# Kernel tuning notes

Measured on AMD Instinct MI355X. Metric: run time of the kernel, lower is better.

## Reference

```python
import jax, jax.numpy as jnp
import numpy as np

B, C, H, W = 4, 256, 64, 64
C8, C2 = C // 8, C // 2


def _conv(x, w, b):
    # NCHW conv with SAME padding
    y = jax.lax.conv_general_dilated(x, w, (1, 1), 'SAME',
                                     dimension_numbers=('NCHW', 'OIHW', 'NCHW'))
    return y + b[None, :, None, None]


def _bn(x, s, bi, m, v):
    # eval-mode batchnorm, eps matches torch default 1e-5
    inv = jax.lax.rsqrt(v + 1e-5)
    return (x - m[None, :, None, None]) * (inv * s)[None, :, None, None] + bi[None, :, None, None]


def setup_inputs() -> dict:
    ks = jax.random.split(jax.random.key(0), 8)
    return {
        'x': jax.random.normal(ks[0], (B, C, H, W), jnp.float32),
        'q_w': jax.random.normal(ks[1], (C8, C, 3, 3), jnp.float32) * 0.02,
        'q_b': jnp.zeros((C8,), jnp.float32),
        'q_bn_s': jnp.ones((C8,), jnp.float32),
        'q_bn_b': jnp.zeros((C8,), jnp.float32),
        'q_bn_m': jnp.zeros((C8,), jnp.float32),
        'q_bn_v': jnp.ones((C8,), jnp.float32),
        'k_w': jax.random.normal(ks[2], (C8, C, 3, 3), jnp.float32) * 0.02,
        'k_b': jnp.zeros((C8,), jnp.float32),
        'k_bn_s': jnp.ones((C8,), jnp.float32),
        'k_bn_b': jnp.zeros((C8,), jnp.float32),
        'k_bn_m': jnp.zeros((C8,), jnp.float32),
        'k_bn_v': jnp.ones((C8,), jnp.float32),
        'v_w': jax.random.normal(ks[3], (C, C), jnp.float32) * 0.02,
        'v_b': jnp.zeros((C,), jnp.float32),
        'gamma': jnp.full((1,), 0.5, jnp.float32),
        'c_w1': jax.random.normal(ks[4], (C2, C), jnp.float32) * 0.02,
        'c_b1': jnp.zeros((C2,), jnp.float32),
        'c_w2': jax.random.normal(ks[5], (C, C2), jnp.float32) * 0.02,
        'c_b2': jnp.zeros((C,), jnp.float32),
        's_vw': jax.random.normal(ks[6], (C, C), jnp.float32) * 0.02,
        's_vb': jnp.zeros((C,), jnp.float32),
        's_cw': jax.random.normal(ks[7], (1, 2, 3, 3), jnp.float32) * 0.1,
        's_cb': jnp.zeros((1,), jnp.float32),
        's_bn_s': jnp.ones((1,), jnp.float32),
        's_bn_b': jnp.zeros((1,), jnp.float32),
        's_bn_m': jnp.zeros((1,), jnp.float32),
        's_bn_v': jnp.ones((1,), jnp.float32),
    }


def reference(x, q_w, q_b, q_bn_s, q_bn_b, q_bn_m, q_bn_v,
              k_w, k_b, k_bn_s, k_bn_b, k_bn_m, k_bn_v,
              v_w, v_b, gamma, c_w1, c_b1, c_w2, c_b2,
              s_vw, s_vb, s_cw, s_cb, s_bn_s, s_bn_b, s_bn_m, s_bn_v):
    Bn, Cn, Hn, Wn = x.shape
    HW = Hn * Wn

    # ---- SelfAttention branch ----
    q = jax.nn.relu(_bn(_conv(x, q_w, q_b), q_bn_s, q_bn_b, q_bn_m, q_bn_v)).reshape(Bn, -1, HW)  # [B,C8,HW]
    k = jax.nn.relu(_bn(_conv(x, k_w, k_b), k_bn_s, k_bn_b, k_bn_m, k_bn_v)).reshape(Bn, -1, HW)  # [B,C8,HW]
    aff = jax.nn.softmax(jnp.einsum('bcn,bcm->bnm', q, k), axis=-1)  # [B,HW,HW]
    v = (jnp.einsum('bchw,oc->bohw', x, v_w) + v_b[None, :, None, None]).reshape(Bn, Cn, HW)
    wts = jnp.einsum('bcm,bnm->bcn', v, aff).reshape(Bn, Cn, Hn, Wn)
    selfA = gamma * wts + x

    # ---- Channel mean/max attention ----
    def fc(s):  # s: [B,C]
        h = jax.nn.relu(s @ c_w1.T + c_b1)
        return h @ c_w2.T + c_b2

    gate = jax.nn.sigmoid(fc(x.mean((2, 3))) + fc(x.max((2, 3))))  # [B,C]
    channelA = x * gate[:, :, None, None]

    # ---- Spatial mean/max attention ----
    v2 = jnp.einsum('bchw,oc->bohw', x, s_vw) + s_vb[None, :, None, None]  # [B,C,H,W]
    sm = jnp.stack([v2.max(1), v2.mean(1)], axis=1)  # [B,2,H,W]
    a = _bn(_conv(sm, s_cw, s_cb), s_bn_s, s_bn_b, s_bn_m, s_bn_v)  # [B,1,H,W]
    a = jax.nn.softmax(a[:, 0], axis=-1)  # [B,H,W], softmax over W
    spatialA = jnp.einsum('bchw,bwk->bchk', x, a)  # batched matmul, needs H==W

    return selfA + channelA + spatialA
```

## Files before the change

### kernel.cpp

```cpp
#include <hip/hip_runtime.h>
#include <math.h>

#define NB 4
#define NC 256
#define NHW 4096
#define NC8 32
#define NC2 128

typedef unsigned short u16;
typedef __attribute__((ext_vector_type(8))) short s8v;
typedef __attribute__((ext_vector_type(4))) short s4v;
typedef __attribute__((ext_vector_type(4))) float f4v;

__device__ __forceinline__ u16 f2bf(float x) {
    unsigned int u = __builtin_bit_cast(unsigned int, x);
    u += 0x7FFFu + ((u >> 16) & 1u);
    return (u16)(u >> 16);
}
__device__ __forceinline__ float bf2f(u16 h) {
    unsigned int u = ((unsigned int)h) << 16;
    return __builtin_bit_cast(float, u);
}
__device__ __forceinline__ s8v ld_sp(const u16* p) {
    s4v a = *(const s4v*)p;
    s4v b = *(const s4v*)(p + 4);
    return __builtin_shufflevector(a, b, 0, 1, 2, 3, 4, 5, 6, 7);
}

#define MFMA16(a, b, c) __builtin_amdgcn_mfma_f32_16x16x32_bf16((a), (b), (c), 0, 0, 0)

__global__ __launch_bounds__(256) void k_conv_qk(
    const float* __restrict__ x,
    const float* __restrict__ qw, const float* __restrict__ kw,
    float* __restrict__ part)
{
    __shared__ float plane[2][64 * 65];
    const int cog = blockIdx.x;
    const int cic = blockIdx.y;
    const int b   = blockIdx.z;
    const int t   = threadIdx.x;
    const int co0 = cog * 4;
    const bool isq = co0 < NC8;
    const int oc0 = isq ? co0 : co0 - NC8;
    const float* wsel = isq ? qw : kw;
    const int ci0 = cic * 64;
    const int r  = t >> 2;
    const int c0 = (t & 3) * 16;
    float acc[4][16];
#pragma unroll
    for (int j = 0; j < 4; ++j)
#pragma unroll
        for (int q = 0; q < 16; ++q) acc[j][q] = 0.f;

    const float* xb = x + (size_t)b * NC * NHW;
    float4 pf[4];
    {
        const float4* src = (const float4*)(xb + (size_t)ci0 * NHW);
#pragma unroll
        for (int u = 0; u < 4; ++u) pf[u] = src[t + 256 * u];
    }
    for (int ci = ci0; ci < ci0 + 64; ++ci) {
        const int cur = ci & 1;
#pragma unroll
        for (int u = 0; u < 4; ++u) {
            int g  = (t + 256 * u) << 2;
            int rr = g >> 6, cc = g & 63;
            float* p = &plane[cur][rr * 65 + cc];
            p[0] = pf[u].x; p[1] = pf[u].y; p[2] = pf[u].z; p[3] = pf[u].w;
        }
        __syncthreads();
        if (ci + 1 < ci0 + 64) {
            const float4* src = (const float4*)(xb + (size_t)(ci + 1) * NHW);
#pragma unroll
            for (int u = 0; u < 4; ++u) pf[u] = src[t + 256 * u];
        }
        float w9[4][9];
#pragma unroll
        for (int j = 0; j < 4; ++j)
#pragma unroll
            for (int u = 0; u < 9; ++u)
                w9[j][u] = wsel[((size_t)(oc0 + j) * NC + ci) * 9 + u];
#pragma unroll
        for (int dy = 0; dy < 3; ++dy) {
            int rr = r + dy - 1;
            if (rr >= 0 && rr <= 63) {
                const float* row = &plane[cur][rr * 65];
                float tv[18];
#pragma unroll
                for (int jj = 0; jj < 18; ++jj) {
                    int cc = c0 + jj - 1;
                    tv[jj] = (cc >= 0 && cc < 64) ? row[cc] : 0.f;
                }
#pragma unroll
                for (int j = 0; j < 4; ++j) {
                    float wa = w9[j][dy * 3 + 0], wb = w9[j][dy * 3 + 1], wc = w9[j][dy * 3 + 2];
#pragma unroll
                    for (int q = 0; q < 16; ++q)
                        acc[j][q] += wa * tv[q] + wb * tv[q + 1] + wc * tv[q + 2];
                }
            }
        }
        __syncthreads();
    }
    float* pp = part + (((size_t)(cic * 4 + b) * 64 + co0) * NHW) + r * 64 + c0;
#pragma unroll
    for (int j = 0; j < 4; ++j)
#pragma unroll
        for (int q4 = 0; q4 < 4; ++q4) {
            float4 o;
            o.x = acc[j][q4 * 4 + 0]; o.y = acc[j][q4 * 4 + 1];
            o.z = acc[j][q4 * 4 + 2]; o.w = acc[j][q4 * 4 + 3];
            *(float4*)(pp + (size_t)j * NHW + q4 * 4) = o;
        }
}

__global__ __launch_bounds__(256) void k_qk_finish(
    const float* __restrict__ part,
    const float* __restrict__ qb, const float* __restrict__ qbs, const float* __restrict__ qbb,
    const float* __restrict__ qbm, const float* __restrict__ qbv,
    const float* __restrict__ kb, const float* __restrict__ kbs, const float* __restrict__ kbb,
    const float* __restrict__ kbm, const float* __restrict__ kbv,
    u16* __restrict__ qh, u16* __restrict__ ql,
    u16* __restrict__ kh, u16* __restrict__ kl)
{
    const int t = threadIdx.x;
    const int b = blockIdx.y;
    const int n = blockIdx.x * 64 + (t & 63);
    const int coq = t >> 6;
    const int cb2 = coq * 16;
    float s[16];
#pragma unroll
    for (int j = 0; j < 16; ++j) s[j] = 0.f;
#pragma unroll
    for (int cic = 0; cic < 4; ++cic)
#pragma unroll
        for (int j = 0; j < 16; ++j)
            s[j] += part[(((size_t)(cic * 4 + b)) * 64 + cb2 + j) * NHW + n];
    const bool isq = coq < 2;
    u16 hi[16], lo[16];
#pragma unroll
    for (int j = 0; j < 16; ++j) {
        int oc = (coq & 1) * 16 + j;
        float cbv = isq ? qb[oc]  : kb[oc];
        float sv  = isq ? qbs[oc] : kbs[oc];
        float bbv = isq ? qbb[oc] : kbb[oc];
        float mv  = isq ? qbm[oc] : kbm[oc];
        float vv  = isq ? qbv[oc] : kbv[oc];
        float inv = rsqrtf(vv + 1e-5f);
        float scale = inv * sv;
        float shift = (cbv - mv) * scale + bbv;
        float y = fmaxf(s[j] * scale + shift, 0.f);
        hi[j] = f2bf(y);
        lo[j] = f2bf(y - bf2f(hi[j]));
    }
    u16* dh = isq ? qh : kh;
    u16* dl = isq ? ql : kl;
    size_t base = ((size_t)b * NHW + n) * 32 + (coq & 1) * 16;
    uint4 ph0, ph1, pl0, pl1;
    ph0.x = (unsigned)hi[0]  | ((unsigned)hi[1]  << 16);
    ph0.y = (unsigned)hi[2]  | ((unsigned)hi[3]  << 16);
    ph0.z = (unsigned)hi[4]  | ((unsigned)hi[5]  << 16);
    ph0.w = (unsigned)hi[6]  | ((unsigned)hi[7]  << 16);
    ph1.x = (unsigned)hi[8]  | ((unsigned)hi[9]  << 16);
    ph1.y = (unsigned)hi[10] | ((unsigned)hi[11] << 16);
    ph1.z = (unsigned)hi[12] | ((unsigned)hi[13] << 16);
    ph1.w = (unsigned)hi[14] | ((unsigned)hi[15] << 16);
    pl0.x = (unsigned)lo[0]  | ((unsigned)lo[1]  << 16);
    pl0.y = (unsigned)lo[2]  | ((unsigned)lo[3]  << 16);
    pl0.z = (unsigned)lo[4]  | ((unsigned)lo[5]  << 16);
    pl0.w = (unsigned)lo[6]  | ((unsigned)lo[7]  << 16);
    pl1.x = (unsigned)lo[8]  | ((unsigned)lo[9]  << 16);
    pl1.y = (unsigned)lo[10] | ((unsigned)lo[11] << 16);
    pl1.z = (unsigned)lo[12] | ((unsigned)lo[13] << 16);
    pl1.w = (unsigned)lo[14] | ((unsigned)lo[15] << 16);
    *(uint4*)&dh[base]     = ph0;
    *(uint4*)&dh[base + 8] = ph1;
    *(uint4*)&dl[base]     = pl0;
    *(uint4*)&dl[base + 8] = pl1;
}

__global__ __launch_bounds__(256) void k_gemm_vv2(
    const float* __restrict__ x,
    const float* __restrict__ vw, const float* __restrict__ vb,
    const float* __restrict__ sw, const float* __restrict__ sb,
    float* __restrict__ v2T, u16* __restrict__ vhi, u16* __restrict__ vlo)
{
    __shared__ float Ax[16 * 68];
    __shared__ float Bw1[16 * 68];
    __shared__ float Bw2[16 * 68];
    const int t  = threadIdx.x;
    const int n0 = blockIdx.x * 64;
    const int o0 = blockIdx.y * 64;
    const int b  = blockIdx.z;
    const int ni = t & 15, oi = t >> 4;
    float a1[4][4], a2[4][4];
#pragma unroll
    for (int i = 0; i < 4; ++i)
#pragma unroll
        for (int j = 0; j < 4; ++j) { a1[i][j] = 0.f; a2[i][j] = 0.f; }

    const int sk  = t >> 4;
    const int sf  = t & 15;
    const int so  = t & 63;
    const int skq = t >> 6;
    const float* xb = x + ((size_t)b * NC) * NHW + n0;

    float4 ax = *(const float4*)(xb + (size_t)sk * NHW + sf * 4);
    float4 f1 = *(const float4*)(vw + (size_t)(o0 + so) * NC + skq * 4);
    float4 f2 = *(const float4*)(sw + (size_t)(o0 + so) * NC + skq * 4);

    for (int c0 = 0; c0 < NC; c0 += 16) {
        *(float4*)&Ax[sk * 68 + sf * 4] = ax;
        Bw1[(skq * 4 + 0) * 68 + so] = f1.x;
        Bw1[(skq * 4 + 1) * 68 + so] = f1.y;
        Bw1[(skq * 4 + 2) * 68 + so] = f1.z;
        Bw1[(skq * 4 + 3) * 68 + so] = f1.w;
        Bw2[(skq * 4 + 0) * 68 + so] = f2.x;
        Bw2[(skq * 4 + 1) * 68 + so] = f2.y;
        Bw2[(skq * 4 + 2) * 68 + so] = f2.z;
        Bw2[(skq * 4 + 3) * 68 + so] = f2.w;
        __syncthreads();
        if (c0 + 16 < NC) {
            ax = *(const float4*)(xb + (size_t)(c0 + 16 + sk) * NHW + sf * 4);
            f1 = *(const float4*)(vw + (size_t)(o0 + so) * NC + c0 + 16 + skq * 4);
            f2 = *(const float4*)(sw + (size_t)(o0 + so) * NC + c0 + 16 + skq * 4);
        }
#pragma unroll
        for (int k = 0; k < 16; ++k) {
            float4 af = *(const float4*)&Ax[k * 68 + ni * 4];
            float4 g1 = *(const float4*)&Bw1[k * 68 + oi * 4];
            float4 g2 = *(const float4*)&Bw2[k * 68 + oi * 4];
            const float* ap = (const float*)&af;
            const float* p1 = (const float*)&g1;
            const float* p2 = (const float*)&g2;
#pragma unroll
            for (int i = 0; i < 4; ++i)
#pragma unroll
                for (int j = 0; j < 4; ++j) {
                    a1[i][j] += ap[i] * p1[j];
                    a2[i][j] += ap[i] * p2[j];
                }
        }
        __syncthreads();
    }
    float vb4[4], sb4[4];
#pragma unroll
    for (int j = 0; j < 4; ++j) { vb4[j] = vb[o0 + oi * 4 + j]; sb4[j] = sb[o0 + oi * 4 + j]; }
#pragma unroll
    for (int i = 0; i < 4; ++i) {
        size_t idx = ((size_t)b * NHW + n0 + ni * 4 + i) * NC + o0 + oi * 4;
        float4 o2v;
        o2v.x = a2[i][0] + sb4[0]; o2v.y = a2[i][1] + sb4[1];
        o2v.z = a2[i][2] + sb4[2]; o2v.w = a2[i][3] + sb4[3];
        *(float4*)&v2T[idx] = o2v;
    }
#pragma unroll
    for (int j = 0; j < 4; ++j) {
        u16 h[4], l[4];
#pragma unroll
        for (int i = 0; i < 4; ++i) {
            float y = a1[i][j] + vb4[j];
            h[i] = f2bf(y);
            l[i] = f2bf(y - bf2f(h[i]));
        }
        size_t vi = ((size_t)b * NC + o0 + oi * 4 + j) * NHW + n0 + ni * 4;
        uint2 uh, ul;
        uh.x = (unsigned)h[0] | ((unsigned)h[1] << 16);
        uh.y = (unsigned)h[2] | ((unsigned)h[3] << 16);
        ul.x = (unsigned)l[0] | ((unsigned)l[1] << 16);
        ul.y = (unsigned)l[2] | ((unsigned)l[3] << 16);
        *(uint2*)&vhi[vi] = uh;
        *(uint2*)&vlo[vi] = ul;
    }
}

__global__ __launch_bounds__(256) void k_reduce_v2(const float* __restrict__ v2T,
                                                   float* __restrict__ smo)
{
    const int t = threadIdx.x;
    const int lane = t & 63, wv = t >> 6;
    const int row = blockIdx.x * 4 + wv;
    float4 f = ((const float4*)(v2T + (size_t)row * NC))[lane];
    float mx = fmaxf(fmaxf(f.x, f.y), fmaxf(f.z, f.w));
    float sm = f.x + f.y + f.z + f.w;
#pragma unroll
    for (int off = 32; off; off >>= 1) {
        mx = fmaxf(mx, __shfl_down(mx, off));
        sm += __shfl_down(sm, off);
    }
    if (lane == 0) {
        int b = row >> 12, n = row & 4095;
        smo[((size_t)b * 2 + 0) * NHW + n] = mx;
        smo[((size_t)b * 2 + 1) * NHW + n] = sm * (1.f / NC);
    }
}

__global__ __launch_bounds__(256) void k_spatial(
    const float* __restrict__ smo, const float* __restrict__ scw,
    const float* __restrict__ scb, const float* __restrict__ sbs,
    const float* __restrict__ sbb2, const float* __restrict__ sbm,
    const float* __restrict__ sbv, float* __restrict__ Amat)
{
    __shared__ float ch[2][64 * 68];
    __shared__ float lg[64 * 68];
    const int t = threadIdx.x;
    const int b = blockIdx.x;
#pragma unroll
    for (int u = 0; u < 8; ++u) {
        int g  = t + 256 * u;
        int c  = g >> 10, gi = g & 1023;
        int row = gi >> 4, col4 = (gi & 15) * 4;
        float4 f = ((const float4*)(smo + ((size_t)b * 2 + c) * NHW))[gi];
        *(float4*)&ch[c][row * 68 + col4] = f;
    }
    __syncthreads();
    float w9[2][9];
#pragma unroll
    for (int ic = 0; ic < 2; ++ic)
#pragma unroll
        for (int j = 0; j < 9; ++j) w9[ic][j] = scw[ic * 9 + j];
    float A0, Bsh;
    {
        float inv = rsqrtf(sbv[0] + 1e-5f);
        A0  = inv * sbs[0];
        Bsh = (scb[0] - sbm[0]) * A0 + sbb2[0];
    }
#pragma unroll
    for (int u = 0; u < 16; ++u) {
        int px = t + 256 * u;
        int h = px >> 6, w = px & 63;
        float acc = 0.f;
#pragma unroll
        for (int ic = 0; ic < 2; ++ic)
#pragma unroll
            for (int dy = 0; dy < 3; ++dy) {
                int rr = h + dy - 1;
                if (rr < 0 || rr > 63) continue;
#pragma unroll
                for (int dx = 0; dx < 3; ++dx) {
                    int cc = w + dx - 1;
                    if (cc < 0 || cc > 63) continue;
                    acc += w9[ic][dy * 3 + dx] * ch[ic][rr * 68 + cc];
                }
            }
        lg[h * 68 + w] = acc * A0 + Bsh;
    }
    __syncthreads();
    if (t < 64) {
        float M = -INFINITY;
        for (int k2 = 0; k2 < 64; ++k2) M = fmaxf(M, lg[t * 68 + k2]);
        float L = 0.f;
        for (int k2 = 0; k2 < 64; ++k2) L += __expf(lg[t * 68 + k2] - M);
        float rli = 1.f / L;
        for (int k2 = 0; k2 < 64; ++k2)
            Amat[(size_t)b * NHW + t * 64 + k2] = __expf(lg[t * 68 + k2] - M) * rli;
    }
}

__global__ __launch_bounds__(256) void k_xstats(const float* __restrict__ x,
                                                float* __restrict__ smean,
                                                float* __restrict__ smax)
{
    const int t = threadIdx.x;
    const int c = blockIdx.x, b = blockIdx.y;
    const float* row = x + ((size_t)b * NC + c) * NHW;
    float s = 0.f, m = -INFINITY;
#pragma unroll
    for (int u = 0; u < 4; ++u) {
        float4 f = ((const float4*)row)[t + 256 * u];
        s += f.x + f.y + f.z + f.w;
        m = fmaxf(m, fmaxf(fmaxf(f.x, f.y), fmaxf(f.z, f.w)));
    }
    __shared__ float red[8];
    const int lane = t & 63, wv = t >> 6;
#pragma unroll
    for (int off = 32; off; off >>= 1) {
        s += __shfl_down(s, off);
        m = fmaxf(m, __shfl_down(m, off));
    }
    if (lane == 0) { red[wv] = s; red[4 + wv] = m; }
    __syncthreads();
    if (t == 0) {
        float S = red[0] + red[1] + red[2] + red[3];
        float M = fmaxf(fmaxf(red[4], red[5]), fmaxf(red[6], red[7]));
        smean[b * NC + c] = S * (1.f / NHW);
        smax[b * NC + c]  = M;
    }
}

__global__ __launch_bounds__(256) void k_gate(
    const float* __restrict__ smean, const float* __restrict__ smax,
    const float* __restrict__ w1, const float* __restrict__ b1,
    const float* __restrict__ w2, const float* __restrict__ b2,
    float* __restrict__ gate)
{
    __shared__ float smL[256], sxL[256], hL[256];
    const int t = threadIdx.x;
    const int b = blockIdx.x;
    smL[t] = smean[b * NC + t];
    sxL[t] = smax[b * NC + t];
    __syncthreads();
    {
        const int j = t & 127;
        const float* in = (t < 128) ? smL : sxL;
        const float* wr = w1 + (size_t)j * NC;
        float acc = b1[j];
        for (int c = 0; c < NC; c += 4) {
            float4 f = *(const float4*)(wr + c);
            acc += f.x * in[c] + f.y * in[c + 1] + f.z * in[c + 2] + f.w * in[c + 3];
        }
        hL[t] = fmaxf(acc, 0.f);
    }
    __syncthreads();
    {
        const float* wr = w2 + (size_t)t * NC2;
        float acc = 2.f * b2[t];
        for (int j = 0; j < NC2; j += 4) {
            float4 f = *(const float4*)(wr + j);
            acc += f.x * (hL[j]     + hL[128 + j])
                 + f.y * (hL[j + 1] + hL[129 + j])
                 + f.z * (hL[j + 2] + hL[130 + j])
                 + f.w * (hL[j + 3] + hL[131 + j]);
        }
        gate[b * NC + t] = 1.f / (1.f + __expf(-acc));
    }
}

__global__ __launch_bounds__(64) void k_softstats(
    const u16* __restrict__ qh, const u16* __restrict__ ql,
    const u16* __restrict__ kh, const u16* __restrict__ kl,
    float* __restrict__ mx, float* __restrict__ rl)
{
    const int t  = threadIdx.x;
    const int li = t & 15, g = t >> 4;
    const int n0 = blockIdx.x * 16;
    const int b  = blockIdx.y;
    const size_t qoff = ((size_t)b * NHW + n0 + li) * 32 + g * 8;
    const s8v qfh = *(const s8v*)&qh[qoff];
    const s8v qfl = *(const s8v*)&ql[qoff];
    const size_t kb0 = ((size_t)b * NHW + li) * 32 + g * 8;
    s8v ka0 = *(const s8v*)&kh[kb0];
    s8v ka1 = *(const s8v*)&kh[kb0 + 512];
    s8v la0 = *(const s8v*)&kl[kb0];
    s8v la1 = *(const s8v*)&kl[kb0 + 512];
    float mrun = -INFINITY, lrun = 0.f;
    for (int it = 0; it < 128; ++it) {
        f4v c0 = {0.f, 0.f, 0.f, 0.f}, c1 = {0.f, 0.f, 0.f, 0.f};
        c0 = MFMA16(ka0, qfh, c0); c0 = MFMA16(ka0, qfl, c0); c0 = MFMA16(la0, qfh, c0);
        c1 = MFMA16(ka1, qfh, c1); c1 = MFMA16(ka1, qfl, c1); c1 = MFMA16(la1, qfh, c1);
        if (it + 1 < 128) {
            size_t o = kb0 + (size_t)(it + 1) * 1024;
            ka0 = *(const s8v*)&kh[o];
            ka1 = *(const s8v*)&kh[o + 512];
            la0 = *(const s8v*)&kl[o];
            la1 = *(const s8v*)&kl[o + 512];
        }
        float tmax = fmaxf(fmaxf(fmaxf(c0[0], c0[1]), fmaxf(c0[2], c0[3])),
                           fmaxf(fmaxf(c1[0], c1[1]), fmaxf(c1[2], c1[3])));
        tmax = fmaxf(tmax, __shfl_xor(tmax, 16));
        tmax = fmaxf(tmax, __shfl_xor(tmax, 32));
        float nm = fmaxf(mrun, tmax);
        float ls = 0.f;
#pragma unroll
        for (int r = 0; r < 4; ++r) ls += __expf(c0[r] - nm);
#pragma unroll
        for (int r = 0; r < 4; ++r) ls += __expf(c1[r] - nm);
        ls += __shfl_xor(ls, 16);
        ls += __shfl_xor(ls, 32);
        lrun = lrun * __expf(mrun - nm) + ls;
        mrun = nm;
    }
    if (g == 0) {
        mx[(size_t)b * NHW + n0 + li] = mrun;
        rl[(size_t)b * NHW + n0 + li] = 1.f / lrun;
    }
}

__global__ __launch_bounds__(256, 2) void k_flash(
    const u16* __restrict__ qh, const u16* __restrict__ ql,
    const u16* __restrict__ kh, const u16* __restrict__ kl,
    const u16* __restrict__ vhi, const u16* __restrict__ vlo,
    const float* __restrict__ mx, const float* __restrict__ rl,
    float* __restrict__ w0, float* __restrict__ w1)
{
    __shared__ __align__(16) u16 Sp[2][4][16 * 36];
    const int t = threadIdx.x;
    const int bid = blockIdx.x;
    const int v   = (bid & 7) * 64 + (bid >> 3);
    const int n0  = (v & 63) * 64;
    const int mh  = (v >> 6) & 1;
    const int b   = v >> 7;
    const int mbase = mh * 2048;
    const int li = t & 15, g = (t >> 4) & 3, wv = t >> 6;

    const size_t qoff = ((size_t)b * NHW + n0 + wv * 16 + li) * 32 + g * 8;
    const s8v qfh = *(const s8v*)&qh[qoff];
    const s8v qfl = *(const s8v*)&ql[qoff];
    const float mxv = mx[(size_t)b * NHW + n0 + wv * 16 + li];
    const float rlv = rl[(size_t)b * NHW + n0 + wv * 16 + li];

    f4v acc[4][4];
#pragma unroll
    for (int i = 0; i < 4; ++i)
#pragma unroll
        for (int j = 0; j < 4; ++j) { f4v z = {0.f, 0.f, 0.f, 0.f}; acc[i][j] = z; }

    const size_t kb0 = ((size_t)b * NHW + mbase + li) * 32 + g * 8;
    s8v ka0 = *(const s8v*)&kh[kb0];
    s8v ka1 = *(const s8v*)&kh[kb0 + 512];
    s8v la0 = *(const s8v*)&kl[kb0];
    s8v la1 = *(const s8v*)&kl[kb0 + 512];

    const size_t vb0 = ((size_t)b * NC + wv * 64 + li) * NHW + mbase + g * 8;
    s8v vfh[4], vfl[4];
#pragma unroll
    for (int ct = 0; ct < 4; ++ct) {
        vfh[ct] = *(const s8v*)&vhi[vb0 + (size_t)ct * 16 * NHW];
        vfl[ct] = *(const s8v*)&vlo[vb0 + (size_t)ct * 16 * NHW];
    }

    for (int it = 0; it < 64; ++it) {
        f4v c0 = {0.f, 0.f, 0.f, 0.f}, c1 = {0.f, 0.f, 0.f, 0.f};
        c0 = MFMA16(ka0, qfh, c0); c0 = MFMA16(ka0, qfl, c0); c0 = MFMA16(la0, qfh, c0);
        c1 = MFMA16(ka1, qfh, c1); c1 = MFMA16(ka1, qfl, c1); c1 = MFMA16(la1, qfh, c1);
        {
            size_t o = kb0 + (size_t)(it + 1) * 1024;
            ka0 = *(const s8v*)&kh[o];
            ka1 = *(const s8v*)&kh[o + 512];
            la0 = *(const s8v*)&kl[o];
            la1 = *(const s8v*)&kl[o + 512];
        }
        u16 h0[4], h1[4];
#pragma unroll
        for (int r = 0; r < 4; ++r) {
            h0[r] = f2bf(__expf(c0[r] - mxv) * rlv);
            h1[r] = f2bf(__expf(c1[r] - mxv) * rlv);
        }
        u16* sp = &Sp[it & 1][wv][0];
        uint2 uw0, uw1;
        uw0.x = (unsigned)h0[0] | ((unsigned)h0[1] << 16);
        uw0.y = (unsigned)h0[2] | ((unsigned)h0[3] << 16);
        uw1.x = (unsigned)h1[0] | ((unsigned)h1[1] << 16);
        uw1.y = (unsigned)h1[2] | ((unsigned)h1[3] << 16);
        *(uint2*)&sp[li * 36 + g * 4]      = uw0;
        *(uint2*)&sp[li * 36 + 16 + g * 4] = uw1;
        __syncthreads();
        s8v pa0 = ld_sp(&Sp[it & 1][0][li * 36 + g * 8]);
        s8v pa1 = ld_sp(&Sp[it & 1][1][li * 36 + g * 8]);
        s8v pa2 = ld_sp(&Sp[it & 1][2][li * 36 + g * 8]);
        s8v pa3 = ld_sp(&Sp[it & 1][3][li * 36 + g * 8]);
#pragma unroll
        for (int ct = 0; ct < 4; ++ct) {
            acc[0][ct] = MFMA16(pa0, vfh[ct], acc[0][ct]);
            acc[0][ct] = MFMA16(pa0, vfl[ct], acc[0][ct]);
            acc[1][ct] = MFMA16(pa1, vfh[ct], acc[1][ct]);
            acc[1][ct] = MFMA16(pa1, vfl[ct], acc[1][ct]);
            acc[2][ct] = MFMA16(pa2, vfh[ct], acc[2][ct]);
            acc[2][ct] = MFMA16(pa2, vfl[ct], acc[2][ct]);
            acc[3][ct] = MFMA16(pa3, vfh[ct], acc[3][ct]);
            acc[3][ct] = MFMA16(pa3, vfl[ct], acc[3][ct]);
        }
        {
            size_t o = vb0 + (size_t)(it + 1) * 32;
#pragma unroll
            for (int ct = 0; ct < 4; ++ct) {
                vfh[ct] = *(const s8v*)&vhi[o + (size_t)ct * 16 * NHW];
                vfl[ct] = *(const s8v*)&vlo[o + (size_t)ct * 16 * NHW];
            }
        }
    }
    float* wout = (mh == 0) ? w0 : w1;
#pragma unroll
    for (int ng = 0; ng < 4; ++ng)
#pragma unroll
        for (int ct = 0; ct < 4; ++ct)
#pragma unroll
            for (int r = 0; r < 4; ++r)
                wout[((size_t)b * NHW + n0 + ng * 16 + g * 4 + r) * NC
                     + wv * 64 + ct * 16 + li] = acc[ng][ct][r];
}

__global__ __launch_bounds__(256) void k_final(
    const float* __restrict__ x, const float* __restrict__ w0,
    const float* __restrict__ w1, const float* __restrict__ gate,
    const float* __restrict__ Amat, const float* __restrict__ gamma,
    float* __restrict__ out)
{
    __shared__ float As[64 * 65];
    __shared__ float xs[64 * 65];
    const int t = threadIdx.x;
    const int h = blockIdx.x, b = blockIdx.y;
    const float g0 = gamma[0];
    const int kq = t >> 4;
    const int cq = t & 15;
#pragma unroll
    for (int u = 0; u < 4; ++u) {
        int gidx = t + 256 * u;
        int w = gidx >> 4, k4 = (gidx & 15) * 4;
        float4 f = ((const float4*)(Amat + (size_t)b * NHW))[gidx];
        *(float4*)&As[w * 65 + k4] = f;
    }
    for (int ch = 0; ch < 4; ++ch) {
        __syncthreads();
#pragma unroll
        for (int u = 0; u < 4; ++u) {
            int gidx = t + 256 * u;
            int c = gidx >> 4, w4 = (gidx & 15) * 4;
            float4 f = *(const float4*)(x + ((size_t)(b * NC) + ch * 64 + c) * NHW + h * 64 + w4);
            xs[(w4 + 0) * 65 + c] = f.x;
            xs[(w4 + 1) * 65 + c] = f.y;
            xs[(w4 + 2) * 65 + c] = f.z;
            xs[(w4 + 3) * 65 + c] = f.w;
        }
        __syncthreads();
        float acc[4][4];
#pragma unroll
        for (int i = 0; i < 4; ++i)
#pragma unroll
            for (int j = 0; j < 4; ++j) acc[i][j] = 0.f;
        for (int w = 0; w < 64; ++w) {
            float4 av = *(const float4*)&As[w * 65 + kq * 4];
            float4 xv = *(const float4*)&xs[w * 65 + cq * 4];
            const float* ap = (const float*)&av;
            const float* xp = (const float*)&xv;
#pragma unroll
            for (int i = 0; i < 4; ++i)
#pragma unroll
                for (int j = 0; j < 4; ++j)
                    acc[i][j] += xp[i] * ap[j];
        }
#pragma unroll
        for (int i = 0; i < 4; ++i) {
            const int c = ch * 64 + cq * 4 + i;
            const float gt1 = 1.f + gate[b * NC + c];
#pragma unroll
            for (int j = 0; j < 4; ++j) {
                const int k = kq * 4 + j;
                const int n = h * 64 + k;
                const float xv = xs[k * 65 + cq * 4 + i];
                const size_t widx = ((size_t)b * NHW + n) * NC + c;
                const float wsum = w0[widx] + w1[widx];
                out[((size_t)(b * NC + c)) * NHW + n] = g0 * wsum + xv * gt1 + acc[i][j];
            }
        }
    }
}

extern "C" void kernel_launch(void* const* d_in, const int* in_sizes, int n_in,
                              void* d_out, int out_size, void* d_ws, size_t ws_size,
                              hipStream_t stream)
{
    const float* x    = (const float*)d_in[0];
    const float* qw   = (const float*)d_in[1];
    const float* qb   = (const float*)d_in[2];
    const float* qbs  = (const float*)d_in[3];
    const float* qbb  = (const float*)d_in[4];
    const float* qbm  = (const float*)d_in[5];
    const float* qbv  = (const float*)d_in[6];
    const float* kw   = (const float*)d_in[7];
    const float* kb   = (const float*)d_in[8];
    const float* kbs  = (const float*)d_in[9];
    const float* kbb  = (const float*)d_in[10];
    const float* kbm  = (const float*)d_in[11];
    const float* kbv  = (const float*)d_in[12];
    const float* vw   = (const float*)d_in[13];
    const float* vb   = (const float*)d_in[14];
    const float* gm   = (const float*)d_in[15];
    const float* cw1  = (const float*)d_in[16];
    const float* cb1  = (const float*)d_in[17];
    const float* cw2  = (const float*)d_in[18];
    const float* cb2  = (const float*)d_in[19];
    const float* svw  = (const float*)d_in[20];
    const float* svb  = (const float*)d_in[21];
    const float* scw  = (const float*)d_in[22];
    const float* scb  = (const float*)d_in[23];
    const float* sbs  = (const float*)d_in[24];
    const float* sbb  = (const float*)d_in[25];
    const float* sbm  = (const float*)d_in[26];
    const float* sbv  = (const float*)d_in[27];

    float* ws    = (float*)d_ws;
    float* part  = ws;
    float* w0    = ws;
    float* v2T   = ws + 4194304;
    float* w1    = ws + 4194304;
    u16*   vhi   = (u16*)(ws + 8388608);
    u16*   vlo   = (u16*)(ws + 10485760);
    u16*   qhB   = (u16*)(ws + 12582912);
    u16*   qlB   = (u16*)(ws + 12845056);
    u16*   khB   = (u16*)(ws + 13107200);
    u16*   klB   = (u16*)(ws + 13369344);
    float* mxp   = ws + 13631488;
    float* rlp   = ws + 13647872;
    float* smean = ws + 13664256;
    float* smax  = ws + 13665280;
    float* gate  = ws + 13666304;
    float* smo   = ws + 13667328;
    float* Amat  = ws + 13700096;

    k_conv_qk  <<<dim3(16, 4, NB), 256, 0, stream>>>(x, qw, kw, part);
    k_qk_finish<<<dim3(64, NB),    256, 0, stream>>>(part, qb, qbs, qbb, qbm, qbv,
                                                     kb, kbs, kbb, kbm, kbv,
                                                     qhB, qlB, khB, klB);
    k_gemm_vv2 <<<dim3(64, 4, NB), 256, 0, stream>>>(x, vw, vb, svw, svb, v2T, vhi, vlo);
    k_reduce_v2<<<dim3(4096),      256, 0, stream>>>(v2T, smo);
    k_spatial  <<<dim3(NB),        256, 0, stream>>>(smo, scw, scb, sbs, sbb, sbm, sbv, Amat);
    k_xstats   <<<dim3(NC, NB),    256, 0, stream>>>(x, smean, smax);
    k_gate     <<<dim3(NB),        256, 0, stream>>>(smean, smax, cw1, cb1, cw2, cb2, gate);
    k_softstats<<<dim3(256, NB),   64,  0, stream>>>(qhB, qlB, khB, klB, mxp, rlp);
    k_flash    <<<dim3(512),       256, 0, stream>>>(qhB, qlB, khB, klB, vhi, vlo,
                                                     mxp, rlp, w0, w1);
    k_final    <<<dim3(64, NB),    256, 0, stream>>>(x, w0, w1, gate, Amat, gm,
                                                     (float*)d_out);
}
```

Before: 533.3 us.

## Warp-specialize flash kernel, split keys four ways, store bf16 partials

```diff
diff --git a/kernel.cpp b/kernel.cpp
--- a/kernel.cpp
+++ b/kernel.cpp
@@ -476,113 +476,128 @@
     }
 }
 
-__global__ __launch_bounds__(256, 2) void k_flash(
+__global__ __launch_bounds__(512, 4) void k_flash(
     const u16* __restrict__ qh, const u16* __restrict__ ql,
     const u16* __restrict__ kh, const u16* __restrict__ kl,
     const u16* __restrict__ vhi, const u16* __restrict__ vlo,
     const float* __restrict__ mx, const float* __restrict__ rl,
-    float* __restrict__ w0, float* __restrict__ w1)
-{
+    u16* __restrict__ w)
+{
+    __shared__ __align__(16) u16 Sk[2][2][32 * 40];
     __shared__ __align__(16) u16 Sp[2][4][16 * 36];
     const int t = threadIdx.x;
     const int bid = blockIdx.x;
-    const int v   = (bid & 7) * 64 + (bid >> 3);
+    const int v   = (bid & 7) * 128 + (bid >> 3);
     const int n0  = (v & 63) * 64;
-    const int mh  = (v >> 6) & 1;
-    const int b   = v >> 7;
-    const int mbase = mh * 2048;
+    const int mh  = (v >> 6) & 3;
+    const int b   = v >> 8;
+    const int mbase = mh * 1024;
     const int li = t & 15, g = (t >> 4) & 3, wv = t >> 6;
-
-    const size_t qoff = ((size_t)b * NHW + n0 + wv * 16 + li) * 32 + g * 8;
-    const s8v qfh = *(const s8v*)&qh[qoff];
-    const s8v qfl = *(const s8v*)&ql[qoff];
-    const float mxv = mx[(size_t)b * NHW + n0 + wv * 16 + li];
-    const float rlv = rl[(size_t)b * NHW + n0 + wv * 16 + li];
-
-    f4v acc[4][4];
-#pragma unroll
-    for (int i = 0; i < 4; ++i)
-#pragma unroll
-        for (int j = 0; j < 4; ++j) { f4v z = {0.f, 0.f, 0.f, 0.f}; acc[i][j] = z; }
-
-    const size_t kb0 = ((size_t)b * NHW + mbase + li) * 32 + g * 8;
-    s8v ka0 = *(const s8v*)&kh[kb0];
-    s8v ka1 = *(const s8v*)&kh[kb0 + 512];
-    s8v la0 = *(const s8v*)&kl[kb0];
-    s8v la1 = *(const s8v*)&kl[kb0 + 512];
-
-    const size_t vb0 = ((size_t)b * NC + wv * 64 + li) * NHW + mbase + g * 8;
-    s8v vfh[4], vfl[4];
-#pragma unroll
-    for (int ct = 0; ct < 4; ++ct) {
+    const bool qkrole = wv < 4;
+
+    s8v qfh = {0,0,0,0,0,0,0,0}, qfl = {0,0,0,0,0,0,0,0};
+    float mxv = 0.f, rlv = 0.f;
+    if (qkrole) {
+        const size_t qoff = ((size_t)b * NHW + n0 + wv * 16 + li) * 32 + g * 8;
+        qfh = *(const s8v*)&qh[qoff];
+        qfl = *(const s8v*)&ql[qoff];
+        mxv = mx[(size_t)b * NHW + n0 + wv * 16 + li];
+        rlv = rl[(size_t)b * NHW + n0 + wv * 16 + li];
+    }
+    const int tid2 = t - 256;
+    const int sel  = (tid2 >> 7) & 1;
+    const int sidx = tid2 & 127;
+    const int smp  = sidx >> 2;
+    const int sc8  = (sidx & 3) * 8;
+    const u16* ksrc = sel ? kl : kh;
+    const size_t kgbase = ((size_t)b * NHW + mbase + smp) * 32 + sc8;
+    s8v kreg = {0,0,0,0,0,0,0,0};
+    if (!qkrole) {
+        kreg = *(const s8v*)&ksrc[kgbase];
+        *(s8v*)&Sk[0][sel][smp * 40 + sc8] = kreg;
+        kreg = *(const s8v*)&ksrc[kgbase + 1024];
+    }
+    const size_t vb0 = ((size_t)b * NC + wv * 32 + li) * NHW + mbase + g * 8;
+    s8v vfh[2], vfl[2];
+#pragma unroll
+    for (int ct = 0; ct < 2; ++ct) {
         vfh[ct] = *(const s8v*)&vhi[vb0 + (size_t)ct * 16 * NHW];
         vfl[ct] = *(const s8v*)&vlo[vb0 + (size_t)ct * 16 * NHW];
     }
-
-    for (int it = 0; it < 64; ++it) {
-        f4v c0 = {0.f, 0.f, 0.f, 0.f}, c1 = {0.f, 0.f, 0.f, 0.f};
-        c0 = MFMA16(ka0, qfh, c0); c0 = MFMA16(ka0, qfl, c0); c0 = MFMA16(la0, qfh, c0);
-        c1 = MFMA16(ka1, qfh, c1); c1 = MFMA16(ka1, qfl, c1); c1 = MFMA16(la1, qfh, c1);
-        {
-            size_t o = kb0 + (size_t)(it + 1) * 1024;
-            ka0 = *(const s8v*)&kh[o];
-            ka1 = *(const s8v*)&kh[o + 512];
-            la0 = *(const s8v*)&kl[o];
-            la1 = *(const s8v*)&kl[o + 512];
-        }
-        u16 h0[4], h1[4];
-#pragma unroll
-        for (int r = 0; r < 4; ++r) {
-            h0[r] = f2bf(__expf(c0[r] - mxv) * rlv);
-            h1[r] = f2bf(__expf(c1[r] - mxv) * rlv);
-        }
-        u16* sp = &Sp[it & 1][wv][0];
-        uint2 uw0, uw1;
-        uw0.x = (unsigned)h0[0] | ((unsigned)h0[1] << 16);
-        uw0.y = (unsigned)h0[2] | ((unsigned)h0[3] << 16);
-        uw1.x = (unsigned)h1[0] | ((unsigned)h1[1] << 16);
-        uw1.y = (unsigned)h1[2] | ((unsigned)h1[3] << 16);
-        *(uint2*)&sp[li * 36 + g * 4]      = uw0;
-        *(uint2*)&sp[li * 36 + 16 + g * 4] = uw1;
-        __syncthreads();
-        s8v pa0 = ld_sp(&Sp[it & 1][0][li * 36 + g * 8]);
-        s8v pa1 = ld_sp(&Sp[it & 1][1][li * 36 + g * 8]);
-        s8v pa2 = ld_sp(&Sp[it & 1][2][li * 36 + g * 8]);
-        s8v pa3 = ld_sp(&Sp[it & 1][3][li * 36 + g * 8]);
-#pragma unroll
-        for (int ct = 0; ct < 4; ++ct) {
-            acc[0][ct] = MFMA16(pa0, vfh[ct], acc[0][ct]);
-            acc[0][ct] = MFMA16(pa0, vfl[ct], acc[0][ct]);
-            acc[1][ct] = MFMA16(pa1, vfh[ct], acc[1][ct]);
-            acc[1][ct] = MFMA16(pa1, vfl[ct], acc[1][ct]);
-            acc[2][ct] = MFMA16(pa2, vfh[ct], acc[2][ct]);
-            acc[2][ct] = MFMA16(pa2, vfl[ct], acc[2][ct]);
-            acc[3][ct] = MFMA16(pa3, vfh[ct], acc[3][ct]);
-            acc[3][ct] = MFMA16(pa3, vfl[ct], acc[3][ct]);
+    f4v acc[4][2];
+#pragma unroll
+    for (int i = 0; i < 4; ++i)
+#pragma unroll
+        for (int j = 0; j < 2; ++j) { f4v z = {0.f, 0.f, 0.f, 0.f}; acc[i][j] = z; }
+
+    __syncthreads();
+
+    for (int it = 0; it < 32; ++it) {
+        if (qkrole) {
+            const u16* skh = &Sk[it & 1][0][0];
+            const u16* skl = &Sk[it & 1][1][0];
+            s8v ka0 = *(const s8v*)&skh[li * 40 + g * 8];
+            s8v ka1 = *(const s8v*)&skh[(16 + li) * 40 + g * 8];
+            s8v la0 = *(const s8v*)&skl[li * 40 + g * 8];
+            s8v la1 = *(const s8v*)&skl[(16 + li) * 40 + g * 8];
+            f4v c0 = {0.f, 0.f, 0.f, 0.f}, c1 = {0.f, 0.f, 0.f, 0.f};
+            c0 = MFMA16(ka0, qfh, c0); c0 = MFMA16(ka0, qfl, c0); c0 = MFMA16(la0, qfh, c0);
+            c1 = MFMA16(ka1, qfh, c1); c1 = MFMA16(ka1, qfl, c1); c1 = MFMA16(la1, qfh, c1);
+            u16 h0[4], h1[4];
+#pragma unroll
+            for (int r = 0; r < 4; ++r) {
+                h0[r] = f2bf(__expf(c0[r] - mxv) * rlv);
+                h1[r] = f2bf(__expf(c1[r] - mxv) * rlv);
+            }
+            u16* sp = &Sp[it & 1][wv][0];
+            uint2 uw0, uw1;
+            uw0.x = (unsigned)h0[0] | ((unsigned)h0[1] << 16);
+            uw0.y = (unsigned)h0[2] | ((unsigned)h0[3] << 16);
+            uw1.x = (unsigned)h1[0] | ((unsigned)h1[1] << 16);
+            uw1.y = (unsigned)h1[2] | ((unsigned)h1[3] << 16);
+            *(uint2*)&sp[li * 36 + g * 4]      = uw0;
+            *(uint2*)&sp[li * 36 + 16 + g * 4] = uw1;
+        } else {
+            *(s8v*)&Sk[(it + 1) & 1][sel][smp * 40 + sc8] = kreg;
+            kreg = *(const s8v*)&ksrc[kgbase + (size_t)(it + 2) * 1024];
+        }
+        asm volatile("s_waitcnt lgkmcnt(0)" ::: "memory");
+        __builtin_amdgcn_s_barrier();
+        asm volatile("" ::: "memory");
+        s8v pa[4];
+#pragma unroll
+        for (int ng = 0; ng < 4; ++ng)
+            pa[ng] = ld_sp(&Sp[it & 1][ng][li * 36 + g * 8]);
+#pragma unroll
+        for (int ng = 0; ng < 4; ++ng) {
+            acc[ng][0] = MFMA16(pa[ng], vfh[0], acc[ng][0]);
+            acc[ng][0] = MFMA16(pa[ng], vfl[0], acc[ng][0]);
+            acc[ng][1] = MFMA16(pa[ng], vfh[1], acc[ng][1]);
+            acc[ng][1] = MFMA16(pa[ng], vfl[1], acc[ng][1]);
         }
         {
             size_t o = vb0 + (size_t)(it + 1) * 32;
 #pragma unroll
-            for (int ct = 0; ct < 4; ++ct) {
+            for (int ct = 0; ct < 2; ++ct) {
                 vfh[ct] = *(const s8v*)&vhi[o + (size_t)ct * 16 * NHW];
                 vfl[ct] = *(const s8v*)&vlo[o + (size_t)ct * 16 * NHW];
             }
         }
     }
-    float* wout = (mh == 0) ? w0 : w1;
+    u16* wout = w + (size_t)mh * 4194304;
 #pragma unroll
     for (int ng = 0; ng < 4; ++ng)
 #pragma unroll
-        for (int ct = 0; ct < 4; ++ct)
+        for (int ct = 0; ct < 2; ++ct)
 #pragma unroll
             for (int r = 0; r < 4; ++r)
                 wout[((size_t)b * NHW + n0 + ng * 16 + g * 4 + r) * NC
-                     + wv * 64 + ct * 16 + li] = acc[ng][ct][r];
+                     + wv * 32 + ct * 16 + li] = f2bf(acc[ng][ct][r]);
 }
 
 __global__ __launch_bounds__(256) void k_final(
-    const float* __restrict__ x, const float* __restrict__ w0,
-    const float* __restrict__ w1, const float* __restrict__ gate,
+    const float* __restrict__ x, const u16* __restrict__ wp,
+    const float* __restrict__ gate,
     const float* __restrict__ Amat, const float* __restrict__ gamma,
     float* __restrict__ out)
 {
@@ -629,18 +644,28 @@
                 for (int j = 0; j < 4; ++j)
                     acc[i][j] += xp[i] * ap[j];
         }
-#pragma unroll
-        for (int i = 0; i < 4; ++i) {
-            const int c = ch * 64 + cq * 4 + i;
-            const float gt1 = 1.f + gate[b * NC + c];
-#pragma unroll
-            for (int j = 0; j < 4; ++j) {
-                const int k = kq * 4 + j;
-                const int n = h * 64 + k;
+        float gt1[4];
+#pragma unroll
+        for (int i = 0; i < 4; ++i) gt1[i] = 1.f + gate[b * NC + ch * 64 + cq * 4 + i];
+#pragma unroll
+        for (int j = 0; j < 4; ++j) {
+            const int k = kq * 4 + j;
+            const int n = h * 64 + k;
+            size_t wb = ((size_t)b * NHW + n) * NC + ch * 64 + cq * 4;
+            float ws4[4] = {0.f, 0.f, 0.f, 0.f};
+#pragma unroll
+            for (int m = 0; m < 4; ++m) {
+                uint2 uw = *(const uint2*)&wp[(size_t)m * 4194304 + wb];
+                ws4[0] += bf2f((u16)(uw.x & 0xffff));
+                ws4[1] += bf2f((u16)(uw.x >> 16));
+                ws4[2] += bf2f((u16)(uw.y & 0xffff));
+                ws4[3] += bf2f((u16)(uw.y >> 16));
+            }
+#pragma unroll
+            for (int i = 0; i < 4; ++i) {
+                const int c = ch * 64 + cq * 4 + i;
                 const float xv = xs[k * 65 + cq * 4 + i];
-                const size_t widx = ((size_t)b * NHW + n) * NC + c;
-                const float wsum = w0[widx] + w1[widx];
-                out[((size_t)(b * NC + c)) * NHW + n] = g0 * wsum + xv * gt1 + acc[i][j];
+                out[((size_t)(b * NC + c)) * NHW + n] = g0 * ws4[i] + xv * gt1[i] + acc[i][j];
             }
         }
     }
@@ -681,9 +706,8 @@
 
     float* ws    = (float*)d_ws;
     float* part  = ws;
-    float* w0    = ws;
     float* v2T   = ws + 4194304;
-    float* w1    = ws + 4194304;
+    u16*   wbf   = (u16*)ws;
     u16*   vhi   = (u16*)(ws + 8388608);
     u16*   vlo   = (u16*)(ws + 10485760);
     u16*   qhB   = (u16*)(ws + 12582912);
@@ -708,8 +732,8 @@
     k_xstats   <<<dim3(NC, NB),    256, 0, stream>>>(x, smean, smax);
     k_gate     <<<dim3(NB),        256, 0, stream>>>(smean, smax, cw1, cb1, cw2, cb2, gate);
     k_softstats<<<dim3(256, NB),   64,  0, stream>>>(qhB, qlB, khB, klB, mxp, rlp);
-    k_flash    <<<dim3(512),       256, 0, stream>>>(qhB, qlB, khB, klB, vhi, vlo,
-                                                     mxp, rlp, w0, w1);
-    k_final    <<<dim3(64, NB),    256, 0, stream>>>(x, w0, w1, gate, Amat, gm,
+    k_flash    <<<dim3(1024),      512, 0, stream>>>(qhB, qlB, khB, klB, vhi, vlo,
+                                                     mxp, rlp, wbf);
+    k_final    <<<dim3(64, NB),    256, 0, stream>>>(x, wbf, gate, Amat, gm,
                                                      (float*)d_out);
 }
```

After: 504.0 us. 5.5% less time.
